# Optimization experiments

Measured on AMD Instinct MI355X. Metric: run time of the kernel, lower is better.

Reference implementation:

```python
import jax, jax.numpy as jnp
import numpy as np

N_HEADS = 16  # matches init_kwargs

def setup_inputs() -> dict:
    key = jax.random.key(0)
    kq, kk, kv = jax.random.split(key, 3)
    B, L, S, D = 4, 2048, 2048, 1024
    queries = jax.random.normal(kq, (B, L, D), dtype=jnp.float32)
    keys = jax.random.normal(kk, (B, S, D), dtype=jnp.float32)
    values = jax.random.normal(kv, (B, S, D), dtype=jnp.float32)
    # TriangularCausalMask: True above the diagonal (positions to mask)
    causal = jnp.triu(jnp.ones((L, S), dtype=bool), k=1)
    attn_mask = jnp.broadcast_to(causal[None, None], (B, 1, L, S))
    return {"queries": queries, "keys": keys, "values": values, "attn_mask": attn_mask}

def reference(queries, keys, values, attn_mask):
    B, L, _ = queries.shape
    S = keys.shape[1]
    H = N_HEADS
    q = queries.reshape(B, L, H, -1)   # (B,L,H,E)
    k = keys.reshape(B, S, H, -1)      # (B,S,H,E)
    v = values.reshape(B, S, H, -1)    # (B,S,H,E)
    scale = 1.0 / jnp.sqrt(jnp.asarray(q.shape[-1], dtype=q.dtype))
    scores = jnp.einsum('blhe,bshe->bhls', q, k)          # (B,H,L,S)
    scores = jnp.where(attn_mask, -jnp.inf, scores)        # masked_fill_
    A = jax.nn.softmax(scale * scores, axis=-1)            # dropout is identity (p=0 / eval)
    V = jnp.einsum('bhls,bshd->blhd', A, v)                # (B,L,H,E)
    return V.reshape(B, L, -1)
```

## Files before the change

### kernel.cpp

```cpp
#include <hip/hip_runtime.h>
#include <hip/hip_bf16.h>

typedef __attribute__((ext_vector_type(8))) short short8;
typedef __attribute__((ext_vector_type(4))) short short4v;
typedef __attribute__((ext_vector_type(4))) float floatx4;

constexpr int B = 4, L = 2048, H = 16, E = 64, D = 1024;
constexpr int STR = 72;
constexpr float SCL_LOG2E = 0.125f * 1.4426950408889634f;

__device__ __forceinline__ short bf16_bits(float x) {
    __hip_bfloat16 b = __float2bfloat16(x);
    return *(const short*)&b;
}

__device__ __forceinline__ short8 packq8(float4 a, float4 c, float scl) {
    short8 r;
    r[0] = bf16_bits(a.x * scl); r[1] = bf16_bits(a.y * scl);
    r[2] = bf16_bits(a.z * scl); r[3] = bf16_bits(a.w * scl);
    r[4] = bf16_bits(c.x * scl); r[5] = bf16_bits(c.y * scl);
    r[6] = bf16_bits(c.z * scl); r[7] = bf16_bits(c.w * scl);
    return r;
}

__device__ __forceinline__ void load_lds16(const short* g, short* l) {
    __builtin_amdgcn_global_load_lds(
        (const __attribute__((address_space(1))) unsigned int*)g,
        (__attribute__((address_space(3))) unsigned int*)l, 16, 0, 0);
}

__global__ __launch_bounds__(256)
void prep_kv(const float* __restrict__ K, const float* __restrict__ V,
             short* __restrict__ Kb, short* __restrict__ Vt)
{
    __shared__ __align__(16) short vt[64 * STR];
    const int tid = threadIdx.x;
    const int bh = blockIdx.x >> 5, kt = blockIdx.x & 31;
    const int b = bh >> 4, h = bh & 15;

    const float* Kp = K + ((size_t)(b * L + kt * 64)) * D + h * E;
    const float* Vp = V + ((size_t)(b * L + kt * 64)) * D + h * E;
    short* Kop = Kb + ((size_t)(bh * 32 + kt)) * 4096;
    short* Vop = Vt + ((size_t)(bh * 32 + kt)) * 4096;

    #pragma unroll
    for (int it = 0; it < 2; ++it) {
        int f = it * 256 + tid;
        int nt = f >> 7, hh = (f >> 6) & 1, qd = (f >> 4) & 3, cc = f & 15;
        int s = nt * 16 + cc, d0 = hh * 32 + qd * 8;
        const float* p = Kp + (size_t)s * D + d0;
        float4 x = *(const float4*)p;
        float4 y = *(const float4*)(p + 4);
        union { short sh[8]; uint4 u; } pk;
        pk.sh[0] = bf16_bits(x.x); pk.sh[1] = bf16_bits(x.y);
        pk.sh[2] = bf16_bits(x.z); pk.sh[3] = bf16_bits(x.w);
        pk.sh[4] = bf16_bits(y.x); pk.sh[5] = bf16_bits(y.y);
        pk.sh[6] = bf16_bits(y.z); pk.sh[7] = bf16_bits(y.w);
        *(uint4*)(Kop + (size_t)f * 8) = pk.u;
    }

    #pragma unroll
    for (int p = 0; p < 4; ++p) {
        int idx = p * 256 + tid;
        int s = idx >> 4, c4 = (idx & 15) * 4;
        float4 g = *(const float4*)(Vp + (size_t)s * D + c4);
        vt[(c4 + 0) * STR + s] = bf16_bits(g.x);
        vt[(c4 + 1) * STR + s] = bf16_bits(g.y);
        vt[(c4 + 2) * STR + s] = bf16_bits(g.z);
        vt[(c4 + 3) * STR + s] = bf16_bits(g.w);
    }
    __syncthreads();

    #pragma unroll
    for (int it = 0; it < 2; ++it) {
        int f16 = it * 256 + tid;
        int f8 = f16 * 2;
        int st = f8 >> 8, dt = (f8 >> 6) & 3, qd = (f8 >> 4) & 3;
        int cA = f8 & 15;
        int dA = dt * 16 + cA, dB = dA + 1;
        int s0 = st * 16 + qd * 4;
        uint2 a = *(const uint2*)&vt[dA * STR + s0];
        uint2 c = *(const uint2*)&vt[dB * STR + s0];
        uint4 u; u.x = a.x; u.y = a.y; u.z = c.x; u.w = c.y;
        *(uint4*)(Vop + (size_t)f16 * 8) = u;
    }
}

__device__ __forceinline__ void frag_step(
    const short* __restrict__ kc, const short* __restrict__ vc,
    short8 qf0, short8 qf1, int m0, int t,
    floatx4 (&o)[4], float& lsum, int c16, int quad, int lane)
{
    short4v pa[4];
    const int rel = m0 + 15 - t * 64;
    if (rel >= 78) {
        #pragma unroll
        for (int nt = 0; nt < 4; ++nt) {
            short8 kb0 = *(const short8*)&kc[nt * 1024 + lane * 8];
            short8 kb1 = *(const short8*)&kc[nt * 1024 + 512 + lane * 8];
            floatx4 acc = (floatx4){0.f, 0.f, 0.f, 0.f};
            acc = __builtin_amdgcn_mfma_f32_16x16x32_bf16(kb0, qf0, acc, 0, 0, 0);
            acc = __builtin_amdgcn_mfma_f32_16x16x32_bf16(kb1, qf1, acc, 0, 0, 0);
            #pragma unroll
            for (int r = 0; r < 4; ++r) {
                float p = exp2f(acc[r]);
                lsum += p;
                pa[nt][r] = bf16_bits(p);
            }
        }
        #pragma unroll
        for (int st = 0; st < 4; ++st) {
            #pragma unroll
            for (int dt = 0; dt < 4; ++dt) {
                short4v vb = *(const short4v*)&vc[(st * 4 + dt) * 256 + lane * 4];
                o[dt] = __builtin_amdgcn_mfma_f32_16x16x16bf16_1k(pa[st], vb, o[dt], 0, 0, 0);
            }
        }
    } else {
        const int cnt = (rel >> 4) >= 3 ? 4 : ((rel >> 4) + 1);
        const int m = m0 + c16;
        #pragma unroll
        for (int nt = 0; nt < 4; ++nt) {
            if (nt < cnt) {
                short8 kb0 = *(const short8*)&kc[nt * 1024 + lane * 8];
                short8 kb1 = *(const short8*)&kc[nt * 1024 + 512 + lane * 8];
                floatx4 acc = (floatx4){0.f, 0.f, 0.f, 0.f};
                acc = __builtin_amdgcn_mfma_f32_16x16x32_bf16(kb0, qf0, acc, 0, 0, 0);
                acc = __builtin_amdgcn_mfma_f32_16x16x32_bf16(kb1, qf1, acc, 0, 0, 0);
                const int s0 = t * 64 + nt * 16 + quad * 4;
                #pragma unroll
                for (int r = 0; r < 4; ++r) {
                    if (s0 + r > m) acc[r] = -__builtin_inff();
                    float p = exp2f(acc[r]);
                    lsum += p;
                    pa[nt][r] = bf16_bits(p);
                }
            }
        }
        #pragma unroll
        for (int st = 0; st < 4; ++st) {
            if (st < cnt) {
                #pragma unroll
                for (int dt = 0; dt < 4; ++dt) {
                    short4v vb = *(const short4v*)&vc[(st * 4 + dt) * 256 + lane * 4];
                    o[dt] = __builtin_amdgcn_mfma_f32_16x16x16bf16_1k(pa[st], vb, o[dt], 0, 0, 0);
                }
            }
        }
    }
}

__device__ __forceinline__ void store_frag(
    float lsum, const floatx4 (&o)[4], float* __restrict__ Op,
    int row_base, int c16, int quad)
{
    lsum += __shfl_xor(lsum, 16);
    lsum += __shfl_xor(lsum, 32);
    const int row0 = row_base + quad * 4;
    #pragma unroll
    for (int r = 0; r < 4; ++r) {
        const float inv = 1.f / __shfl(lsum, quad * 4 + r);
        #pragma unroll
        for (int dt = 0; dt < 4; ++dt)
            Op[(size_t)(row0 + r) * D + dt * 16 + c16] = o[dt][r] * inv;
    }
}

__global__ __launch_bounds__(512, 4)
void attn_fwd_p(const float* __restrict__ Q, const short* __restrict__ Kb,
                const short* __restrict__ Vt, float* __restrict__ O)
{
    __shared__ __align__(16) short k_s[2 * 4096];
    __shared__ __align__(16) short v_s[2 * 4096];

    const int tid  = threadIdx.x;
    const int wave = tid >> 6;
    const int lane = tid & 63;
    const int c16  = lane & 15;
    const int quad = lane >> 4;

    const int i  = (int)blockIdx.x;
    const int bh = ((i >> 6) << 3) | (i & 7);
    const int pr = (i >> 3) & 7;
    const int b  = bh >> 4;
    const int h  = bh & 15;

    const float* Qp  = Q  + ((size_t)b * L) * D + h * E;
    const short* Kbp = Kb + ((size_t)bh * 32) * 4096;
    const short* Vtp = Vt + ((size_t)bh * 32) * 4096;
    float*       Op  = O  + ((size_t)b * L) * D + h * E;

    const int qtA = 15 - pr, qtB = pr;
    const int nA  = 2 * qtA + 2;
    const int mA  = qtA * 128 + wave * 16;
    const int mB  = qtB * 128 + wave * 16;

    const float* qra = Qp + (size_t)(mA + c16) * D + quad * 8;
    short8 qfA0 = packq8(*(const float4*)(qra),      *(const float4*)(qra + 4),  SCL_LOG2E);
    short8 qfA1 = packq8(*(const float4*)(qra + 32), *(const float4*)(qra + 36), SCL_LOG2E);
    const float* qrb = Qp + (size_t)(mB + c16) * D + quad * 8;
    short8 qfB0 = packq8(*(const float4*)(qrb),      *(const float4*)(qrb + 4),  SCL_LOG2E);
    short8 qfB1 = packq8(*(const float4*)(qrb + 32), *(const float4*)(qrb + 36), SCL_LOG2E);

    load_lds16(Kbp + (size_t)tid * 8, k_s + wave * 512);
    load_lds16(Vtp + (size_t)tid * 8, v_s + wave * 512);

    floatx4 oA[4], oB[4];
    #pragma unroll
    for (int dt = 0; dt < 4; ++dt) {
        oA[dt] = (floatx4){0.f, 0.f, 0.f, 0.f};
        oB[dt] = (floatx4){0.f, 0.f, 0.f, 0.f};
    }
    float lA = 0.f, lB = 0.f;

    for (int t = 0; t < nA; ++t) {
        __syncthreads();
        const short* kc = k_s + (t & 1) * 4096;
        const short* vc = v_s + (t & 1) * 4096;

        if (t + 1 < nA) {
            const size_t nb = (size_t)(t + 1) * 4096 + (size_t)tid * 8;
            short* kn = k_s + ((t + 1) & 1) * 4096 + wave * 512;
            short* vn = v_s + ((t + 1) & 1) * 4096 + wave * 512;
            load_lds16(Kbp + nb, kn);
            load_lds16(Vtp + nb, vn);
        }

        __builtin_amdgcn_s_setprio(1);
        if (t * 64 <= mA + 15)
            frag_step(kc, vc, qfA0, qfA1, mA, t, oA, lA, c16, quad, lane);
        if (t * 64 <= mB + 15)
            frag_step(kc, vc, qfB0, qfB1, mB, t, oB, lB, c16, quad, lane);
        __builtin_amdgcn_s_setprio(0);
    }

    store_frag(lA, oA, Op, mA, c16, quad);
    store_frag(lB, oB, Op, mB, c16, quad);
}

__global__ __launch_bounds__(256, 2)
void attn_fwd_fb(const float* __restrict__ Q, const float* __restrict__ K,
                 const float* __restrict__ V, float* __restrict__ O)
{
    constexpr int FSTR = 72;
    constexpr int FQT = 64;
    __shared__ __align__(16) short q_s[FQT * FSTR];
    __shared__ __align__(16) short k_s[64 * FSTR];
    __shared__ __align__(16) short vt_s[E * FSTR];
    __shared__ __align__(16) short p_s[4][16 * FSTR];

    const int tid  = threadIdx.x;
    const int wave = tid >> 6;
    const int lane = tid & 63;
    const int c16  = lane & 15;
    const int quad = lane >> 4;

    const int nqt = L / FQT;
    const int qt  = (nqt - 1) - (int)(blockIdx.x % nqt);
    const int bh  = blockIdx.x / nqt;
    const int b   = bh >> 4;
    const int h   = bh & 15;
    const int q_base = qt * FQT;

    const float* Qp = Q + ((size_t)b * L) * D + h * E;
    const float* Kp = K + ((size_t)b * L) * D + h * E;
    const float* Vp = V + ((size_t)b * L) * D + h * E;
    float*       Op = O + ((size_t)b * L) * D + h * E;

    #pragma unroll
    for (int p = 0; p < 4; ++p) {
        int idx = p * 256 + tid;
        int r = idx >> 4, c4 = (idx & 15) * 4;
        float4 f = *(const float4*)(Qp + (size_t)(q_base + r) * D + c4);
        union { short s[4]; uint2 u; } pk;
        pk.s[0] = bf16_bits(f.x); pk.s[1] = bf16_bits(f.y);
        pk.s[2] = bf16_bits(f.z); pk.s[3] = bf16_bits(f.w);
        *(uint2*)&q_s[r * FSTR + c4] = pk.u;
    }
    __syncthreads();

    short8 qf0 = *(const short8*)&q_s[(wave * 16 + c16) * FSTR + quad * 8];
    short8 qf1 = *(const short8*)&q_s[(wave * 16 + c16) * FSTR + 32 + quad * 8];

    floatx4 o_acc[4];
    #pragma unroll
    for (int nt = 0; nt < 4; ++nt) o_acc[nt] = (floatx4){0.f, 0.f, 0.f, 0.f};
    float m_run[4], l_run[4];
    #pragma unroll
    for (int r = 0; r < 4; ++r) { m_run[r] = -__builtin_inff(); l_run[r] = 0.f; }

    for (int t = 0; t <= qt; ++t) {
        const int k_base = t * 64;
        __syncthreads();
        #pragma unroll
        for (int p = 0; p < 4; ++p) {
            int idx = p * 256 + tid;
            int r = idx >> 4, c4 = (idx & 15) * 4;
            float4 f = *(const float4*)(Kp + (size_t)(k_base + r) * D + c4);
            union { short s[4]; uint2 u; } pk;
            pk.s[0] = bf16_bits(f.x); pk.s[1] = bf16_bits(f.y);
            pk.s[2] = bf16_bits(f.z); pk.s[3] = bf16_bits(f.w);
            *(uint2*)&k_s[r * FSTR + c4] = pk.u;
        }
        #pragma unroll
        for (int p = 0; p < 4; ++p) {
            int s  = lane;
            int dg = p * 4 + wave;
            float4 f = *(const float4*)(Vp + (size_t)(k_base + s) * D + dg * 4);
            vt_s[(dg * 4 + 0) * FSTR + s] = bf16_bits(f.x);
            vt_s[(dg * 4 + 1) * FSTR + s] = bf16_bits(f.y);
            vt_s[(dg * 4 + 2) * FSTR + s] = bf16_bits(f.z);
            vt_s[(dg * 4 + 3) * FSTR + s] = bf16_bits(f.w);
        }
        __syncthreads();

        floatx4 sc[4];
        #pragma unroll
        for (int nt = 0; nt < 4; ++nt) {
            floatx4 acc = (floatx4){0.f, 0.f, 0.f, 0.f};
            short8 b0 = *(const short8*)&k_s[(nt * 16 + c16) * FSTR + quad * 8];
            short8 b1 = *(const short8*)&k_s[(nt * 16 + c16) * FSTR + 32 + quad * 8];
            acc = __builtin_amdgcn_mfma_f32_16x16x32_bf16(qf0, b0, acc, 0, 0, 0);
            acc = __builtin_amdgcn_mfma_f32_16x16x32_bf16(qf1, b1, acc, 0, 0, 0);
            sc[nt] = acc;
        }

        const int q_row0 = q_base + wave * 16 + quad * 4;
        #pragma unroll
        for (int nt = 0; nt < 4; ++nt) {
            const int k_col = k_base + nt * 16 + c16;
            #pragma unroll
            for (int r = 0; r < 4; ++r) {
                float s = sc[nt][r] * SCL_LOG2E;
                sc[nt][r] = (k_col <= q_row0 + r) ? s : -__builtin_inff();
            }
        }

        float alpha[4];
        #pragma unroll
        for (int r = 0; r < 4; ++r) {
            float mx = fmaxf(fmaxf(sc[0][r], sc[1][r]), fmaxf(sc[2][r], sc[3][r]));
            mx = fmaxf(mx, __shfl_xor(mx, 1));
            mx = fmaxf(mx, __shfl_xor(mx, 2));
            mx = fmaxf(mx, __shfl_xor(mx, 4));
            mx = fmaxf(mx, __shfl_xor(mx, 8));
            const float m_new = fmaxf(m_run[r], mx);
            alpha[r] = exp2f(m_run[r] - m_new);
            m_run[r] = m_new;
        }
        float psum[4] = {0.f, 0.f, 0.f, 0.f};
        #pragma unroll
        for (int nt = 0; nt < 4; ++nt) {
            #pragma unroll
            for (int r = 0; r < 4; ++r) {
                float p = exp2f(sc[nt][r] - m_run[r]);
                sc[nt][r] = p;
                psum[r] += p;
            }
        }
        #pragma unroll
        for (int r = 0; r < 4; ++r) {
            float s = psum[r];
            s += __shfl_xor(s, 1);
            s += __shfl_xor(s, 2);
            s += __shfl_xor(s, 4);
            s += __shfl_xor(s, 8);
            l_run[r] = l_run[r] * alpha[r] + s;
            #pragma unroll
            for (int nt = 0; nt < 4; ++nt) o_acc[nt][r] *= alpha[r];
        }

        short* pw = &p_s[wave][0];
        #pragma unroll
        for (int nt = 0; nt < 4; ++nt) {
            #pragma unroll
            for (int r = 0; r < 4; ++r)
                pw[(quad * 4 + r) * FSTR + nt * 16 + c16] = bf16_bits(sc[nt][r]);
        }
        __syncthreads();

        #pragma unroll
        for (int kc = 0; kc < 2; ++kc) {
            short8 pa = *(const short8*)&pw[c16 * FSTR + kc * 32 + quad * 8];
            #pragma unroll
            for (int nt = 0; nt < 4; ++nt) {
                short8 vb = *(const short8*)&vt_s[(nt * 16 + c16) * FSTR + kc * 32 + quad * 8];
                o_acc[nt] = __builtin_amdgcn_mfma_f32_16x16x32_bf16(pa, vb, o_acc[nt], 0, 0, 0);
            }
        }
    }

    const int q_row0 = q_base + wave * 16 + quad * 4;
    #pragma unroll
    for (int r = 0; r < 4; ++r) {
        const float inv_l = 1.f / l_run[r];
        #pragma unroll
        for (int nt = 0; nt < 4; ++nt)
            Op[(size_t)(q_row0 + r) * D + nt * 16 + c16] = o_acc[nt][r] * inv_l;
    }
}

extern "C" void kernel_launch(void* const* d_in, const int* in_sizes, int n_in,
                              void* d_out, int out_size, void* d_ws, size_t ws_size,
                              hipStream_t stream)
{
    const float* Q = (const float*)d_in[0];
    const float* K = (const float*)d_in[1];
    const float* V = (const float*)d_in[2];
    float* O = (float*)d_out;

    const size_t elems = (size_t)B * H * L * E;
    const size_t need  = 2 * elems * sizeof(short);

    if (ws_size >= need) {
        short* Kb = (short*)d_ws;
        short* Vt = Kb + elems;
        prep_kv<<<dim3(B * H * 32), dim3(256), 0, stream>>>(K, V, Kb, Vt);
        attn_fwd_p<<<dim3(B * H * 8), dim3(512), 0, stream>>>(Q, Kb, Vt, O);
    } else {
        attn_fwd_fb<<<dim3(B * H * (L / 64)), dim3(256), 0, stream>>>(Q, K, V, O);
    }
}
```

Measured before the change: 227.6 us.

## Halve query tile per block and merge paired-tile steps to share K/V fragments

Each block now has 4 waves (256 threads) covering a 64-row query tile pair, so the grid doubles to 1024 blocks with finer-grained causal load balancing. When both the A and B query tiles are active, a merged step loads each K/V LDS fragment once and issues MFMAs for both tiles, halving LDS reads in that phase. Diagonal masking is limited to the last 16-column subtile, and exp2f is replaced by the hardware exp2 builtin. The trade-off is more blocks, each reloading K/V from global memory, and higher register pressure in the merged path.

```diff
diff --git a/kernel.cpp b/kernel.cpp
--- a/kernel.cpp
+++ b/kernel.cpp
@@ -86,66 +86,92 @@
     }
 }
 
-__device__ __forceinline__ void frag_step(
+__device__ __forceinline__ void step_single(
     const short* __restrict__ kc, const short* __restrict__ vc,
-    short8 qf0, short8 qf1, int m0, int t,
-    floatx4 (&o)[4], float& lsum, int c16, int quad, int lane)
+    short8 qf0, short8 qf1, int mrow, int s_base, int cnt, bool diag,
+    floatx4 (&o)[4], float& lsum, int lane)
 {
     short4v pa[4];
-    const int rel = m0 + 15 - t * 64;
-    if (rel >= 78) {
-        #pragma unroll
-        for (int nt = 0; nt < 4; ++nt) {
+    #pragma unroll
+    for (int nt = 0; nt < 4; ++nt) {
+        if (nt < cnt) {
             short8 kb0 = *(const short8*)&kc[nt * 1024 + lane * 8];
             short8 kb1 = *(const short8*)&kc[nt * 1024 + 512 + lane * 8];
             floatx4 acc = (floatx4){0.f, 0.f, 0.f, 0.f};
             acc = __builtin_amdgcn_mfma_f32_16x16x32_bf16(kb0, qf0, acc, 0, 0, 0);
             acc = __builtin_amdgcn_mfma_f32_16x16x32_bf16(kb1, qf1, acc, 0, 0, 0);
+            if (diag && nt == cnt - 1) {
+                const int s0 = s_base + nt * 16;
+                #pragma unroll
+                for (int r = 0; r < 4; ++r)
+                    if (s0 + r > mrow) acc[r] = -__builtin_inff();
+            }
             #pragma unroll
             for (int r = 0; r < 4; ++r) {
-                float p = exp2f(acc[r]);
+                float p = __builtin_amdgcn_exp2f(acc[r]);
                 lsum += p;
                 pa[nt][r] = bf16_bits(p);
             }
         }
-        #pragma unroll
-        for (int st = 0; st < 4; ++st) {
+    }
+    #pragma unroll
+    for (int st = 0; st < 4; ++st) {
+        if (st < cnt) {
             #pragma unroll
             for (int dt = 0; dt < 4; ++dt) {
                 short4v vb = *(const short4v*)&vc[(st * 4 + dt) * 256 + lane * 4];
                 o[dt] = __builtin_amdgcn_mfma_f32_16x16x16bf16_1k(pa[st], vb, o[dt], 0, 0, 0);
             }
         }
-    } else {
-        const int cnt = (rel >> 4) >= 3 ? 4 : ((rel >> 4) + 1);
-        const int m = m0 + c16;
-        #pragma unroll
-        for (int nt = 0; nt < 4; ++nt) {
-            if (nt < cnt) {
-                short8 kb0 = *(const short8*)&kc[nt * 1024 + lane * 8];
-                short8 kb1 = *(const short8*)&kc[nt * 1024 + 512 + lane * 8];
-                floatx4 acc = (floatx4){0.f, 0.f, 0.f, 0.f};
-                acc = __builtin_amdgcn_mfma_f32_16x16x32_bf16(kb0, qf0, acc, 0, 0, 0);
-                acc = __builtin_amdgcn_mfma_f32_16x16x32_bf16(kb1, qf1, acc, 0, 0, 0);
-                const int s0 = t * 64 + nt * 16 + quad * 4;
+    }
+}
+
+__device__ __forceinline__ void step_merged(
+    const short* __restrict__ kc, const short* __restrict__ vc,
+    short8 qfA0, short8 qfA1, short8 qfB0, short8 qfB1,
+    int mrowB, int s_base, int cntB, bool diagB,
+    floatx4 (&oA)[4], floatx4 (&oB)[4], float& lA, float& lB, int lane)
+{
+    short4v paA[4], paB[4];
+    #pragma unroll
+    for (int nt = 0; nt < 4; ++nt) {
+        short8 kb0 = *(const short8*)&kc[nt * 1024 + lane * 8];
+        short8 kb1 = *(const short8*)&kc[nt * 1024 + 512 + lane * 8];
+        floatx4 a = (floatx4){0.f, 0.f, 0.f, 0.f};
+        a = __builtin_amdgcn_mfma_f32_16x16x32_bf16(kb0, qfA0, a, 0, 0, 0);
+        a = __builtin_amdgcn_mfma_f32_16x16x32_bf16(kb1, qfA1, a, 0, 0, 0);
+        #pragma unroll
+        for (int r = 0; r < 4; ++r) {
+            float p = __builtin_amdgcn_exp2f(a[r]);
+            lA += p;
+            paA[nt][r] = bf16_bits(p);
+        }
+        if (nt < cntB) {
+            floatx4 bb = (floatx4){0.f, 0.f, 0.f, 0.f};
+            bb = __builtin_amdgcn_mfma_f32_16x16x32_bf16(kb0, qfB0, bb, 0, 0, 0);
+            bb = __builtin_amdgcn_mfma_f32_16x16x32_bf16(kb1, qfB1, bb, 0, 0, 0);
+            if (diagB && nt == cntB - 1) {
+                const int s0 = s_base + nt * 16;
                 #pragma unroll
-                for (int r = 0; r < 4; ++r) {
-                    if (s0 + r > m) acc[r] = -__builtin_inff();
-                    float p = exp2f(acc[r]);
-                    lsum += p;
-                    pa[nt][r] = bf16_bits(p);
-                }
-            }
-        }
-        #pragma unroll
-        for (int st = 0; st < 4; ++st) {
-            if (st < cnt) {
-                #pragma unroll
-                for (int dt = 0; dt < 4; ++dt) {
-                    short4v vb = *(const short4v*)&vc[(st * 4 + dt) * 256 + lane * 4];
-                    o[dt] = __builtin_amdgcn_mfma_f32_16x16x16bf16_1k(pa[st], vb, o[dt], 0, 0, 0);
-                }
-            }
+                for (int r = 0; r < 4; ++r)
+                    if (s0 + r > mrowB) bb[r] = -__builtin_inff();
+            }
+            #pragma unroll
+            for (int r = 0; r < 4; ++r) {
+                float p = __builtin_amdgcn_exp2f(bb[r]);
+                lB += p;
+                paB[nt][r] = bf16_bits(p);
+            }
+        }
+    }
+    #pragma unroll
+    for (int st = 0; st < 4; ++st) {
+        #pragma unroll
+        for (int dt = 0; dt < 4; ++dt) {
+            short4v vb = *(const short4v*)&vc[(st * 4 + dt) * 256 + lane * 4];
+            oA[dt] = __builtin_amdgcn_mfma_f32_16x16x16bf16_1k(paA[st], vb, oA[dt], 0, 0, 0);
+            if (st < cntB)
+                oB[dt] = __builtin_amdgcn_mfma_f32_16x16x16bf16_1k(paB[st], vb, oB[dt], 0, 0, 0);
         }
     }
 }
@@ -166,7 +192,7 @@
     }
 }
 
-__global__ __launch_bounds__(512, 4)
+__global__ __launch_bounds__(256, 4)
 void attn_fwd_p(const float* __restrict__ Q, const short* __restrict__ Kb,
                 const short* __restrict__ Vt, float* __restrict__ O)
 {
@@ -180,8 +206,8 @@
     const int quad = lane >> 4;
 
     const int i  = (int)blockIdx.x;
-    const int bh = ((i >> 6) << 3) | (i & 7);
-    const int pr = (i >> 3) & 7;
+    const int bh = ((i >> 7) << 3) | (i & 7);
+    const int pp = (i >> 3) & 15;
     const int b  = bh >> 4;
     const int h  = bh & 15;
 
@@ -190,10 +216,10 @@
     const short* Vtp = Vt + ((size_t)bh * 32) * 4096;
     float*       Op  = O  + ((size_t)b * L) * D + h * E;
 
-    const int qtA = 15 - pr, qtB = pr;
-    const int nA  = 2 * qtA + 2;
-    const int mA  = qtA * 128 + wave * 16;
-    const int mB  = qtB * 128 + wave * 16;
+    const int qtA = 31 - pp, qtB = pp;
+    const int nA  = qtA + 1;
+    const int mA  = qtA * 64 + wave * 16;
+    const int mB  = qtB * 64 + wave * 16;
 
     const float* qra = Qp + (size_t)(mA + c16) * D + quad * 8;
     short8 qfA0 = packq8(*(const float4*)(qra),      *(const float4*)(qra + 4),  SCL_LOG2E);
@@ -202,8 +228,12 @@
     short8 qfB0 = packq8(*(const float4*)(qrb),      *(const float4*)(qrb + 4),  SCL_LOG2E);
     short8 qfB1 = packq8(*(const float4*)(qrb + 32), *(const float4*)(qrb + 36), SCL_LOG2E);
 
-    load_lds16(Kbp + (size_t)tid * 8, k_s + wave * 512);
-    load_lds16(Vtp + (size_t)tid * 8, v_s + wave * 512);
+    #pragma unroll
+    for (int it = 0; it < 2; ++it) {
+        int c = it * 256 + tid;
+        load_lds16(Kbp + (size_t)c * 8, k_s + c * 8);
+        load_lds16(Vtp + (size_t)c * 8, v_s + c * 8);
+    }
 
     floatx4 oA[4], oB[4];
     #pragma unroll
@@ -219,18 +249,30 @@
         const short* vc = v_s + (t & 1) * 4096;
 
         if (t + 1 < nA) {
-            const size_t nb = (size_t)(t + 1) * 4096 + (size_t)tid * 8;
-            short* kn = k_s + ((t + 1) & 1) * 4096 + wave * 512;
-            short* vn = v_s + ((t + 1) & 1) * 4096 + wave * 512;
-            load_lds16(Kbp + nb, kn);
-            load_lds16(Vtp + nb, vn);
+            const size_t nb = (size_t)(t + 1) * 4096;
+            short* kn = k_s + ((t + 1) & 1) * 4096;
+            short* vn = v_s + ((t + 1) & 1) * 4096;
+            #pragma unroll
+            for (int it = 0; it < 2; ++it) {
+                int c = it * 256 + tid;
+                load_lds16(Kbp + nb + (size_t)c * 8, kn + c * 8);
+                load_lds16(Vtp + nb + (size_t)c * 8, vn + c * 8);
+            }
         }
 
         __builtin_amdgcn_s_setprio(1);
-        if (t * 64 <= mA + 15)
-            frag_step(kc, vc, qfA0, qfA1, mA, t, oA, lA, c16, quad, lane);
-        if (t * 64 <= mB + 15)
-            frag_step(kc, vc, qfB0, qfB1, mB, t, oB, lB, c16, quad, lane);
+        const int sb = t * 64 + quad * 4;
+        if (t < qtB) {
+            step_merged(kc, vc, qfA0, qfA1, qfB0, qfB1, 0, sb, 4, false,
+                        oA, oB, lA, lB, lane);
+        } else if (t == qtB) {
+            step_merged(kc, vc, qfA0, qfA1, qfB0, qfB1, mB + c16, sb, wave + 1, true,
+                        oA, oB, lA, lB, lane);
+        } else if (t < qtA) {
+            step_single(kc, vc, qfA0, qfA1, 0, sb, 4, false, oA, lA, lane);
+        } else {
+            step_single(kc, vc, qfA0, qfA1, mA + c16, sb, wave + 1, true, oA, lA, lane);
+        }
         __builtin_amdgcn_s_setprio(0);
     }
 
@@ -416,7 +458,7 @@
         short* Kb = (short*)d_ws;
         short* Vt = Kb + elems;
         prep_kv<<<dim3(B * H * 32), dim3(256), 0, stream>>>(K, V, Kb, Vt);
-        attn_fwd_p<<<dim3(B * H * 8), dim3(512), 0, stream>>>(Q, Kb, Vt, O);
+        attn_fwd_p<<<dim3(B * H * 16), dim3(256), 0, stream>>>(Q, Kb, Vt, O);
     } else {
         attn_fwd_fb<<<dim3(B * H * (L / 64)), dim3(256), 0, stream>>>(Q, K, V, O);
     }
```

Measured after the change: 242.5 us. +6.6%, slower.
